# Kernel tuning notes

Measured on AMD Instinct MI355X. Metric: run time of the kernel, lower is better.

## Reference

```python
import jax, jax.numpy as jnp
import numpy as np

B, S, D, H = 4, 2048, 1024, 16
HD = D // H

def setup_inputs() -> dict:
    key = jax.random.key(0)
    k1, k2, k3 = jax.random.split(key, 3)
    x = jax.random.normal(k1, (B, S, D), dtype=jnp.float32)
    W_qkv = jax.random.normal(k2, (D, 3 * D), dtype=jnp.float32) * (1.0 / np.sqrt(D))
    W_out = jax.random.normal(k3, (D, D), dtype=jnp.float32) * (1.0 / np.sqrt(D))
    causal_mask = jnp.tril(jnp.ones((S, S), dtype=bool))[None, None]  # [1,1,S,S]
    return {"x": x, "causal_mask": causal_mask, "W_qkv": W_qkv, "W_out": W_out}

def reference(x, causal_mask, W_qkv, W_out):
    b, s, d = x.shape
    scale = 1.0 / np.sqrt(HD)
    qkv = x @ W_qkv  # [b,s,3d]
    q, k, v = jnp.split(qkv, 3, axis=-1)
    # [b,h,s,hd]
    q = q.reshape(b, s, H, HD).transpose(0, 2, 1, 3)
    k = k.reshape(b, s, H, HD).transpose(0, 2, 1, 3)
    v = v.reshape(b, s, H, HD).transpose(0, 2, 1, 3)
    scores = jnp.einsum('bhqd,bhkd->bhqk', q, k) * scale
    scores = jnp.where(causal_mask, scores, -jnp.inf)
    attn = jax.nn.softmax(scores, axis=-1)
    out = jnp.einsum('bhqk,bhkd->bhqd', attn, v)
    out = out.transpose(0, 2, 1, 3).reshape(b, s, d)
    return out @ W_out
```

## Files before the change

kernel.cpp:

```cpp
#include <hip/hip_runtime.h>
#include <hip/hip_bf16.h>

typedef __bf16 bf16;
typedef unsigned short u16;
typedef unsigned int u32;
typedef __attribute__((ext_vector_type(8))) __bf16 bf16x8;
typedef __attribute__((ext_vector_type(4))) unsigned short u16x4;
typedef __attribute__((ext_vector_type(4))) float f32x4;

#define B_  4
#define S_  2048
#define D_  1024
#define H_  16
#define HD_ 64

#define QSCALE 0.18033688f

__device__ inline u16 bf16_bits(float f) {
  bf16 h = (bf16)f;
  return __builtin_bit_cast(u16, h);
}

__device__ __forceinline__ void glds16(const bf16* g, bf16* s) {
  __builtin_amdgcn_global_load_lds(
      (const __attribute__((address_space(1))) void*)g,
      (__attribute__((address_space(3))) void*)s, 16, 0, 0);
}

#define MEMFENCE() asm volatile("" ::: "memory")
#define BARRIER_RAW() __builtin_amdgcn_s_barrier()
#define LGKM0() asm volatile("s_waitcnt lgkmcnt(0)" ::: "memory")
#define VMCNT(n) asm volatile("s_waitcnt vmcnt(" #n ")" ::: "memory")

__global__ void cvt_x(const float* __restrict__ in, bf16* __restrict__ out, long n) {
  long i = ((long)blockIdx.x * 256 + threadIdx.x) * 8;
  if (i < n) {
    f32x4 a = *(const f32x4*)(in + i);
    f32x4 b = *(const f32x4*)(in + i + 4);
    bf16x8 v;
#pragma unroll
    for (int j = 0; j < 4; ++j) { v[j] = (bf16)a[j]; v[4 + j] = (bf16)b[j]; }
    *(bf16x8*)(out + i) = v;
  }
}

__global__ void cvt_w(const float* __restrict__ in, bf16* __restrict__ out,
                      int K, int N) {
  __shared__ float tile[32][33];
  int n0 = blockIdx.x * 32, k0 = blockIdx.y * 32;
  int x = threadIdx.x, y = threadIdx.y;
#pragma unroll
  for (int i = 0; i < 32; i += 8)
    tile[y + i][x] = in[(long)(k0 + y + i) * N + (n0 + x)];
  __syncthreads();
#pragma unroll
  for (int i = 0; i < 32; i += 8)
    out[(long)(n0 + y + i) * K + (k0 + x)] = (bf16)tile[x][y + i];
}

template <typename TC>
__launch_bounds__(256)
__global__ void gemm128(const bf16* __restrict__ A, const bf16* __restrict__ Bt,
                        TC* __restrict__ C, int M, int N, int K) {
  __shared__ __attribute__((aligned(16))) bf16 As[8][512];
  __shared__ __attribute__((aligned(16))) bf16 Bs[8][512];
  int t = threadIdx.x;
  int w = t >> 6, lane = t & 63;
  int wr = w >> 1, wc = w & 1;
  int fr = lane & 15, fq = lane >> 4;
  long m0 = (long)blockIdx.y * 128, n0 = (long)blockIdx.x * 128;
  f32x4 acc[4][4] = {};
  const bf16* ag = A  + (m0 + (2 * w) * 16 + fr) * (long)K + fq * 8;
  const bf16* bg = Bt + (n0 + (2 * w) * 16 + fr) * (long)K + fq * 8;
  bf16* al0 = &As[2 * w][0];
  bf16* al1 = &As[2 * w + 1][0];
  bf16* bl0 = &Bs[2 * w][0];
  bf16* bl1 = &Bs[2 * w + 1][0];
  const long K16 = 16 * (long)K;
  for (int k0 = 0; k0 < K; k0 += 32) {
    __syncthreads();
    glds16(ag + k0, al0);
    glds16(ag + k0 + K16, al1);
    glds16(bg + k0, bl0);
    glds16(bg + k0 + K16, bl1);
    __syncthreads();
    bf16x8 af[4], bfv[4];
#pragma unroll
    for (int i = 0; i < 4; ++i) {
      af[i]  = *(const bf16x8*)&As[wr * 4 + i][lane * 8];
      bfv[i] = *(const bf16x8*)&Bs[wc * 4 + i][lane * 8];
    }
#pragma unroll
    for (int mb = 0; mb < 4; ++mb)
#pragma unroll
      for (int nb = 0; nb < 4; ++nb)
        acc[mb][nb] = __builtin_amdgcn_mfma_f32_16x16x32_bf16(
            af[mb], bfv[nb], acc[mb][nb], 0, 0, 0);
  }
#pragma unroll
  for (int mb = 0; mb < 4; ++mb) {
    long row = m0 + wr * 64 + mb * 16 + fq * 4;
#pragma unroll
    for (int nb = 0; nb < 4; ++nb) {
      long col = n0 + wc * 64 + nb * 16 + fr;
#pragma unroll
      for (int i = 0; i < 4; ++i)
        C[(row + i) * (long)N + col] = (TC)acc[mb][nb][i];
    }
  }
}

#define QUAD(HM, HN)                                                          \
  do {                                                                        \
    _Pragma("unroll") for (int m2 = 0; m2 < 4; ++m2) {                        \
      _Pragma("unroll") for (int n2 = 0; n2 < 2; ++n2) {                      \
        _Pragma("unroll") for (int kc = 0; kc < 2; ++kc)                      \
            acc[(HM) * 4 + m2][(HN) * 2 + n2] =                               \
                __builtin_amdgcn_mfma_f32_16x16x32_bf16(                      \
                    aF[m2][kc], bF[(HN) * 2 + n2][kc],                        \
                    acc[(HM) * 4 + m2][(HN) * 2 + n2], 0, 0, 0);              \
      }                                                                       \
    }                                                                         \
  } while (0)

__launch_bounds__(512, 2)
__global__ void gemm_qkv(const bf16* __restrict__ A, const bf16* __restrict__ Bt,
                         bf16* __restrict__ qk, bf16* __restrict__ vT) {
  __shared__ __attribute__((aligned(16))) bf16 smem[2][4][8192];
  const int K = 1024;
  int t = threadIdx.x;
  int w = t >> 6, lane = t & 63;
  int wm = w >> 2, wn = w & 3;
  int fr = lane & 15, fq = lane >> 4;
  long m0 = (long)blockIdx.y * 256, n0 = (long)blockIdx.x * 256;

  {
  }
  int o = t * 16;
  int p = o ^ (((o >> 9) & 1) << 5);
  int si = p >> 10;
  int srow = (si >> 1) * 16 + ((p & 1023) >> 6);
  int scol = (si & 1) * 32 + ((p & 63) >> 1);
  const bf16* aS = A  + (m0 + srow) * (long)K + scol;
  const bf16* bS = Bt + (n0 + srow) * (long)K + scol;

  int fro = (fr << 6) + (fq << 4);
  fro ^= (fr & 8) << 2;
  const char* Afr0 = (const char*)&smem[0][wm][0] + fro;
  const char* Bfr0 = (const char*)&smem[0][2 + (wn >> 1)][0] + ((wn & 1) << 13) + fro;
  bf16* s00 = &smem[0][0][0];

  f32x4 acc[8][4] = {};
  bf16x8 aF[4][2], bF[4][2];

#define STAGE(src, dstRegion)                          \
  do {                                                 \
    glds16((src), (dstRegion) + w * 512);              \
    glds16((src) + 65536, (dstRegion) + 4096 + w * 512); \
  } while (0)

  STAGE(aS,               s00);
  STAGE(aS + 131072,      s00 + 8192);
  STAGE(bS,               s00 + 16384);
  STAGE(bS + 131072,      s00 + 24576);
  STAGE(bS + 64,          s00 + 32768 + 16384);
  STAGE(bS + 64 + 131072, s00 + 32768 + 24576);
  VMCNT(4);
  MEMFENCE(); BARRIER_RAW(); MEMFENCE();

  for (int j = 0; j < 16; ++j) {
    int b = j & 1, nb = b ^ 1;
    long kA = (long)((j + 1 < 16) ? j + 1 : 15) * 64;
    long kB = (long)((j + 2 < 16) ? j + 2 : 15) * 64;
    const char* Ab = Afr0 + b * 65536;
    const char* Bb = Bfr0 + b * 65536;
    bf16* sA0 = s00 + nb * 32768;
    bf16* sB0 = s00 + b * 32768 + 16384;

#pragma unroll
    for (int m2 = 0; m2 < 4; ++m2)
#pragma unroll
      for (int kc = 0; kc < 2; ++kc)
        aF[m2][kc] = *(const bf16x8*)(Ab + (m2 * 2 + kc) * 1024);
#pragma unroll
    for (int n2 = 0; n2 < 2; ++n2)
#pragma unroll
      for (int kc = 0; kc < 2; ++kc)
        bF[n2][kc] = *(const bf16x8*)(Bb + (n2 * 2 + kc) * 1024);
    STAGE(aS + kA, sA0);
    MEMFENCE(); BARRIER_RAW(); LGKM0();
    __builtin_amdgcn_s_setprio(1);
    QUAD(0, 0);
    __builtin_amdgcn_s_setprio(0);
    MEMFENCE(); BARRIER_RAW(); MEMFENCE();

#pragma unroll
    for (int n2 = 2; n2 < 4; ++n2)
#pragma unroll
      for (int kc = 0; kc < 2; ++kc)
        bF[n2][kc] = *(const bf16x8*)(Bb + (n2 * 2 + kc) * 1024);
    STAGE(aS + kA + 131072, sA0 + 8192);
    MEMFENCE(); BARRIER_RAW(); LGKM0();
    __builtin_amdgcn_s_setprio(1);
    QUAD(0, 1);
    __builtin_amdgcn_s_setprio(0);
    MEMFENCE(); BARRIER_RAW(); MEMFENCE();

#pragma unroll
    for (int m2 = 0; m2 < 4; ++m2)
#pragma unroll
      for (int kc = 0; kc < 2; ++kc)
        aF[m2][kc] = *(const bf16x8*)(Ab + ((4 + m2) * 2 + kc) * 1024);
    STAGE(bS + kB, sB0);
    MEMFENCE(); BARRIER_RAW(); LGKM0();
    __builtin_amdgcn_s_setprio(1);
    QUAD(1, 1);
    __builtin_amdgcn_s_setprio(0);
    MEMFENCE(); BARRIER_RAW(); MEMFENCE();

    STAGE(bS + kB + 131072, sB0 + 8192);
    MEMFENCE(); BARRIER_RAW(); LGKM0();
    __builtin_amdgcn_s_setprio(1);
    QUAD(1, 0);
    __builtin_amdgcn_s_setprio(0);
    VMCNT(4);
    MEMFENCE(); BARRIER_RAW(); MEMFENCE();
  }
#undef STAGE

#pragma unroll
  for (int fm = 0; fm < 8; ++fm) {
    long row = m0 + wm * 128 + fm * 16 + fq * 4;
    long bb = row >> 11;
    long s0 = row & 2047;
#pragma unroll
    for (int fn = 0; fn < 4; ++fn) {
      long col = n0 + wn * 64 + fn * 16 + fr;
      if (col < 2048) {
        float sc = (col < 1024) ? QSCALE : 1.f;
#pragma unroll
        for (int i = 0; i < 4; ++i)
          qk[(row + i) * 2048 + col] = (bf16)(acc[fm][fn][i] * sc);
      } else {
        u16x4 pk;
#pragma unroll
        for (int i = 0; i < 4; ++i) pk[i] = bf16_bits(acc[fm][fn][i]);
        *(u16x4*)(vT + (bb * 1024 + (col - 2048)) * 2048 + s0) = pk;
      }
    }
  }
}

__launch_bounds__(256, 2)
__global__ void attn_mfma3(const bf16* __restrict__ qk, const bf16* __restrict__ vT,
                           bf16* __restrict__ out) {
  __shared__ __attribute__((aligned(16))) bf16 Ks[4][2][512];
  __shared__ __attribute__((aligned(16))) bf16 Vs[4][2][512];
  __shared__ __attribute__((aligned(16))) bf16 Pb[4][16][76];
  int pr = blockIdx.x, h = blockIdx.y, b = blockIdx.z;
  int t = threadIdx.x, w = t >> 6, lane = t & 63;
  int fr = lane & 15, fq = lane >> 4;
  const bf16* qkb = qk + (long)b * S_ * 2048;
  const bf16* vTb = vT + ((long)b * 1024 + h * HD_) * 2048;
  bf16* ob = out + (long)b * S_ * D_ + h * HD_;

  for (int half = 0; half < 2; ++half) {
    int st = half ? (15 - pr) : pr;
    int qbase = st * 128 + w * 32;
    bf16x8 aQ[2][2];
#pragma unroll
    for (int s = 0; s < 2; ++s)
#pragma unroll
      for (int kc = 0; kc < 2; ++kc)
        aQ[s][kc] = *(const bf16x8*)(qkb + (long)(qbase + s * 16 + fr) * 2048 +
                                     h * HD_ + kc * 32 + fq * 8);
    f32x4 acc_o[2][4] = {};
    float lsum[2][4] = {};
    int jtmax = 2 * st + 1;

    for (int jt = 0; jt <= jtmax; ++jt) {
      __syncthreads();
      {
        const bf16* kg = qkb + (long)(jt * 64 + w * 16 + fr) * 2048 + 1024 + h * HD_ + fq * 8;
        glds16(kg,      &Ks[w][0][0]);
        glds16(kg + 32, &Ks[w][1][0]);
        const bf16* vg = vTb + (long)(w * 16 + fr) * 2048 + jt * 64 + fq * 8;
        glds16(vg,      &Vs[w][0][0]);
        glds16(vg + 32, &Vs[w][1][0]);
      }
      __syncthreads();
      bf16x8 bK[4][2], bV[4][2];
#pragma unroll
      for (int nb = 0; nb < 4; ++nb)
#pragma unroll
        for (int kc = 0; kc < 2; ++kc) {
          bK[nb][kc] = *(const bf16x8*)&Ks[nb][kc][lane * 8];
          bV[nb][kc] = *(const bf16x8*)&Vs[nb][kc][lane * 8];
        }
#pragma unroll
      for (int s = 0; s < 2; ++s) {
        int dlim = qbase + s * 16 - jt * 64;
        if (dlim <= -16) continue;
        f32x4 acc_s[4] = {};
#pragma unroll
        for (int nb = 0; nb < 4; ++nb) {
          acc_s[nb] = __builtin_amdgcn_mfma_f32_16x16x32_bf16(aQ[s][0], bK[nb][0], acc_s[nb], 0, 0, 0);
          acc_s[nb] = __builtin_amdgcn_mfma_f32_16x16x32_bf16(aQ[s][1], bK[nb][1], acc_s[nb], 0, 0, 0);
        }
        if (dlim < 63) {
#pragma unroll
          for (int i = 0; i < 4; ++i) {
            int qa = dlim + fq * 4 + i;
#pragma unroll
            for (int nb = 0; nb < 4; ++nb) {
              float pv = exp2f(acc_s[nb][i]);
              if (nb * 16 + fr > qa) pv = 0.f;
              lsum[s][i] += pv;
              Pb[w][fq * 4 + i][nb * 16 + fr] = (bf16)pv;
            }
          }
        } else {
#pragma unroll
          for (int i = 0; i < 4; ++i)
#pragma unroll
            for (int nb = 0; nb < 4; ++nb) {
              float pv = exp2f(acc_s[nb][i]);
              lsum[s][i] += pv;
              Pb[w][fq * 4 + i][nb * 16 + fr] = (bf16)pv;
            }
        }
#pragma unroll
        for (int kc = 0; kc < 2; ++kc) {
          bf16x8 aP = *(const bf16x8*)&Pb[w][fr][kc * 32 + fq * 8];
#pragma unroll
          for (int nb = 0; nb < 4; ++nb)
            acc_o[s][nb] = __builtin_amdgcn_mfma_f32_16x16x32_bf16(aP, bV[nb][kc], acc_o[s][nb], 0, 0, 0);
        }
      }
    }
#pragma unroll
    for (int s = 0; s < 2; ++s) {
      long r0 = (long)(qbase + s * 16 + fq * 4);
#pragma unroll
      for (int i = 0; i < 4; ++i) {
        float l = lsum[s][i];
#pragma unroll
        for (int d = 1; d < 16; d <<= 1) l += __shfl_xor(l, d, 16);
        float inv = 1.f / l;
#pragma unroll
        for (int nb = 0; nb < 4; ++nb)
          ob[(r0 + i) * D_ + nb * 16 + fr] = (bf16)(acc_o[s][nb][i] * inv);
      }
    }
  }
}

__global__ void sentinel_k(float* out, float v, int n) {
  int i = blockIdx.x * 256 + threadIdx.x;
  if (i < n) out[i] = v;
}

extern "C" void kernel_launch(void* const* d_in, const int* in_sizes, int n_in,
                              void* d_out, int out_size, void* d_ws, size_t ws_size,
                              hipStream_t stream) {
  const float* x    = (const float*)d_in[0];
  const float* Wqkv = (const float*)d_in[2];
  const float* Wout = (const float*)d_in[3];
  float* out = (float*)d_out;

  const size_t SD = (size_t)S_ * D_;
  bf16* qk     = (bf16*)d_ws;
  bf16* vT     = qk + (size_t)8192 * 2048;
  bf16* x_bf   = vT + (size_t)4 * 1024 * 2048;
  bf16* ao     = x_bf;
  bf16* wqkv_t = x_bf + (size_t)8192 * 1024;
  bf16* wout_t = wqkv_t + (size_t)3072 * 1024;
  size_t need = ((size_t)16777216 + 8388608 + 8388608 + 3145728 + 1048576) * sizeof(bf16);

  if (ws_size >= need) {
    cvt_x<<<4096, 256, 0, stream>>>(x, x_bf, (long)(B_ * SD));
    cvt_w<<<dim3(3072 / 32, 1024 / 32), dim3(32, 8), 0, stream>>>(Wqkv, wqkv_t, 1024, 3072);
    cvt_w<<<dim3(1024 / 32, 1024 / 32), dim3(32, 8), 0, stream>>>(Wout, wout_t, 1024, 1024);
    gemm_qkv<<<dim3(3072 / 256, (B_ * S_) / 256), 512, 0, stream>>>(
        x_bf, wqkv_t, qk, vT);
    attn_mfma3<<<dim3(8, H_, B_), 256, 0, stream>>>(qk, vT, ao);
    gemm128<float><<<dim3(D_ / 128, (B_ * S_) / 128), 256, 0, stream>>>(
        ao, wout_t, out, B_ * S_, D_, D_);
  } else {
    float v = 1000.f + (float)(ws_size >> 20);
    int n = (int)((size_t)B_ * SD);
    sentinel_k<<<(n + 255) / 256, 256, 0, stream>>>(out, v, n);
  }
}
```

Measured before the change: 299.1 us.

## Double-buffer K/V tiles in attention and compute row sums via MFMA

```diff
diff --git a/kernel.cpp b/kernel.cpp
--- a/kernel.cpp
+++ b/kernel.cpp
@@ -134,8 +134,6 @@
   int fr = lane & 15, fq = lane >> 4;
   long m0 = (long)blockIdx.y * 256, n0 = (long)blockIdx.x * 256;
 
-  {
-  }
   int o = t * 16;
   int p = o ^ (((o >> 9) & 1) << 5);
   int si = p >> 10;
@@ -254,8 +252,8 @@
 __launch_bounds__(256, 2)
 __global__ void attn_mfma3(const bf16* __restrict__ qk, const bf16* __restrict__ vT,
                            bf16* __restrict__ out) {
-  __shared__ __attribute__((aligned(16))) bf16 Ks[4][2][512];
-  __shared__ __attribute__((aligned(16))) bf16 Vs[4][2][512];
+  __shared__ __attribute__((aligned(16))) bf16 Ks[2][4][2][512];
+  __shared__ __attribute__((aligned(16))) bf16 Vs[2][4][2][512];
   __shared__ __attribute__((aligned(16))) bf16 Pb[4][16][76];
   int pr = blockIdx.x, h = blockIdx.y, b = blockIdx.z;
   int t = threadIdx.x, w = t >> 6, lane = t & 63;
@@ -264,9 +262,24 @@
   const bf16* vTb = vT + ((long)b * 1024 + h * HD_) * 2048;
   bf16* ob = out + (long)b * S_ * D_ + h * HD_;
 
+  bf16x8 ones;
+#pragma unroll
+  for (int j = 0; j < 8; ++j) ones[j] = (bf16)1.0f;
+
+  const bf16* kg0 = qkb + (long)(w * 16 + fr) * 2048 + 1024 + h * HD_ + fq * 8;
+  const bf16* vg0 = vTb + (long)(w * 16 + fr) * 2048 + fq * 8;
+
   for (int half = 0; half < 2; ++half) {
     int st = half ? (15 - pr) : pr;
     int qbase = st * 128 + w * 32;
+    int jtmax = 2 * st + 1;
+
+    __syncthreads();
+    glds16(kg0,      &Ks[0][w][0][0]);
+    glds16(kg0 + 32, &Ks[0][w][1][0]);
+    glds16(vg0,      &Vs[0][w][0][0]);
+    glds16(vg0 + 32, &Vs[0][w][1][0]);
+
     bf16x8 aQ[2][2];
 #pragma unroll
     for (int s = 0; s < 2; ++s)
@@ -275,27 +288,27 @@
         aQ[s][kc] = *(const bf16x8*)(qkb + (long)(qbase + s * 16 + fr) * 2048 +
                                      h * HD_ + kc * 32 + fq * 8);
     f32x4 acc_o[2][4] = {};
-    float lsum[2][4] = {};
-    int jtmax = 2 * st + 1;
+    f32x4 acc_l[2] = {};
 
     for (int jt = 0; jt <= jtmax; ++jt) {
+      int c = jt & 1;
       __syncthreads();
-      {
-        const bf16* kg = qkb + (long)(jt * 64 + w * 16 + fr) * 2048 + 1024 + h * HD_ + fq * 8;
-        glds16(kg,      &Ks[w][0][0]);
-        glds16(kg + 32, &Ks[w][1][0]);
-        const bf16* vg = vTb + (long)(w * 16 + fr) * 2048 + jt * 64 + fq * 8;
-        glds16(vg,      &Vs[w][0][0]);
-        glds16(vg + 32, &Vs[w][1][0]);
+      if (jt < jtmax) {
+        int n = c ^ 1;
+        const bf16* kg = kg0 + (long)(jt + 1) * 64 * 2048;
+        const bf16* vg = vg0 + (jt + 1) * 64;
+        glds16(kg,      &Ks[n][w][0][0]);
+        glds16(kg + 32, &Ks[n][w][1][0]);
+        glds16(vg,      &Vs[n][w][0][0]);
+        glds16(vg + 32, &Vs[n][w][1][0]);
       }
-      __syncthreads();
       bf16x8 bK[4][2], bV[4][2];
 #pragma unroll
       for (int nb = 0; nb < 4; ++nb)
 #pragma unroll
         for (int kc = 0; kc < 2; ++kc) {
-          bK[nb][kc] = *(const bf16x8*)&Ks[nb][kc][lane * 8];
-          bV[nb][kc] = *(const bf16x8*)&Vs[nb][kc][lane * 8];
+          bK[nb][kc] = *(const bf16x8*)&Ks[c][nb][kc][lane * 8];
+          bV[nb][kc] = *(const bf16x8*)&Vs[c][nb][kc][lane * 8];
         }
 #pragma unroll
       for (int s = 0; s < 2; ++s) {
@@ -315,7 +328,6 @@
             for (int nb = 0; nb < 4; ++nb) {
               float pv = exp2f(acc_s[nb][i]);
               if (nb * 16 + fr > qa) pv = 0.f;
-              lsum[s][i] += pv;
               Pb[w][fq * 4 + i][nb * 16 + fr] = (bf16)pv;
             }
           }
@@ -325,13 +337,13 @@
 #pragma unroll
             for (int nb = 0; nb < 4; ++nb) {
               float pv = exp2f(acc_s[nb][i]);
-              lsum[s][i] += pv;
               Pb[w][fq * 4 + i][nb * 16 + fr] = (bf16)pv;
             }
         }
 #pragma unroll
         for (int kc = 0; kc < 2; ++kc) {
           bf16x8 aP = *(const bf16x8*)&Pb[w][fr][kc * 32 + fq * 8];
+          acc_l[s] = __builtin_amdgcn_mfma_f32_16x16x32_bf16(aP, ones, acc_l[s], 0, 0, 0);
 #pragma unroll
           for (int nb = 0; nb < 4; ++nb)
             acc_o[s][nb] = __builtin_amdgcn_mfma_f32_16x16x32_bf16(aP, bV[nb][kc], acc_o[s][nb], 0, 0, 0);
@@ -343,10 +355,7 @@
       long r0 = (long)(qbase + s * 16 + fq * 4);
 #pragma unroll
       for (int i = 0; i < 4; ++i) {
-        float l = lsum[s][i];
-#pragma unroll
-        for (int d = 1; d < 16; d <<= 1) l += __shfl_xor(l, d, 16);
-        float inv = 1.f / l;
+        float inv = 1.f / acc_l[s][i];
 #pragma unroll
         for (int nb = 0; nb < 4; ++nb)
           ob[(r0 + i) * D_ + nb * 16 + fr] = (bf16)(acc_o[s][nb][i] * inv);
```

After: 296.0 us. Within noise of the previous version (-1.1%).
